# Performance work log

Hardware: AMD Instinct MI355X
Metric: run time of the kernel (lower is better)

## Reference

```python
import jax, jax.numpy as jnp
import numpy as np

N_NODES = 100000
N_EDGES = 1000000
IN_DIM, HID_DIM, OUT_DIM = 64, 64, 128


def gcn_conv(x, W, b, src, dst, deg_inv_sqrt, n_nodes):
    # PyG GCNConv: x' = D^{-1/2} (A + I) D^{-1/2} (x W) + b
    xw = x @ W  # [N, out]
    norm = deg_inv_sqrt[src] * deg_inv_sqrt[dst]  # [E'] (edges incl. self-loops)
    msgs = xw[src] * norm[:, None]  # gather + scale, [E', out]
    out = jax.ops.segment_sum(msgs, dst, num_segments=n_nodes)
    return out + b


def setup_inputs() -> dict:
    key = jax.random.key(0)
    ks = jax.random.split(key, 8)
    x = jax.random.normal(ks[0], (N_NODES, IN_DIM), dtype=jnp.float32)
    edge_index = jax.random.randint(ks[1], (2, N_EDGES), 0, N_NODES, dtype=jnp.int64 if jax.config.read('jax_enable_x64') else jnp.int32)
    # Glorot-ish init for weights, zeros for biases (matches GCNConv defaults)
    def glorot(k, fan_in, fan_out):
        s = jnp.sqrt(6.0 / (fan_in + fan_out))
        return jax.random.uniform(k, (fan_in, fan_out), jnp.float32, -s, s)
    return {
        "x": x,
        "W1": glorot(ks[2], IN_DIM, HID_DIM), "b1": jnp.zeros((HID_DIM,), jnp.float32),
        "W2": glorot(ks[3], HID_DIM, HID_DIM), "b2": jnp.zeros((HID_DIM,), jnp.float32),
        "W3": glorot(ks[4], HID_DIM, OUT_DIM), "b3": jnp.zeros((OUT_DIM,), jnp.float32),
        "edge_index": edge_index,
    }


def reference(x, W1, b1, W2, b2, W3, b3, edge_index):
    n = x.shape[0]
    loop = jnp.arange(n, dtype=edge_index.dtype)
    src = jnp.concatenate([edge_index[0], loop])  # add self-loops
    dst = jnp.concatenate([edge_index[1], loop])
    deg = jax.ops.segment_sum(jnp.ones_like(dst, dtype=x.dtype), dst, num_segments=n)
    deg_inv_sqrt = jnp.where(deg > 0, jax.lax.rsqrt(deg), 0.0)
    # Dropout(p=0.5) is identity in eval mode
    h = jax.nn.relu(gcn_conv(x, W1, b1, src, dst, deg_inv_sqrt, n))
    h = jax.nn.relu(gcn_conv(h, W2, b2, src, dst, deg_inv_sqrt, n))
    return gcn_conv(h, W3, b3, src, dst, deg_inv_sqrt, n)
```

## Files before the change

### kernel.cpp

```cpp
#include <hip/hip_runtime.h>
#include <hip/hip_fp16.h>


#define NBMAX 512
#define EPB   4096


__global__ __launch_bounds__(256) void bin_hist(const int* __restrict__ dst,
                                                int* __restrict__ hist, int E, int NB) {
  __shared__ int cnt[NBMAX];
  for (int i = threadIdx.x; i < NB; i += 256) cnt[i] = 0;
  __syncthreads();
  int base = blockIdx.x * EPB;
  for (int it = 0; it < EPB; it += 256) {
    int e = base + it + threadIdx.x;
    if (e < E) atomicAdd(&cnt[dst[e] >> 8], 1);
  }
  __syncthreads();
  for (int i = threadIdx.x; i < NB; i += 256) hist[(size_t)blockIdx.x * NB + i] = cnt[i];
}

__global__ __launch_bounds__(256) void bucket_prefix(int* __restrict__ hist,
                                                     int* __restrict__ bucket_tot,
                                                     int nblk, int NB) {
  __shared__ int tmp[256];
  int b = blockIdx.x;
  int t = threadIdx.x;
  int v = (t < nblk) ? hist[(size_t)t * NB + b] : 0;
  tmp[t] = v;
  __syncthreads();
  for (int off = 1; off < 256; off <<= 1) {
    int a = (t >= off) ? tmp[t - off] : 0;
    __syncthreads();
    tmp[t] += a;
    __syncthreads();
  }
  if (t < nblk) hist[(size_t)t * NB + b] = tmp[t] - v;
  if (t == 255) bucket_tot[b] = tmp[255];
}

__global__ __launch_bounds__(512) void bucket_scan(const int* __restrict__ bucket_tot,
                                                   int* __restrict__ bucket_off, int NB, int E) {
  __shared__ int tmp[NBMAX];
  int t = threadIdx.x;
  int v = (t < NB) ? bucket_tot[t] : 0;
  tmp[t] = v;
  __syncthreads();
  for (int off = 1; off < 512; off <<= 1) {
    int a = (t >= off) ? tmp[t - off] : 0;
    __syncthreads();
    tmp[t] += a;
    __syncthreads();
  }
  if (t < NB) bucket_off[t] = tmp[t] - v;
  if (t == 0) bucket_off[NB] = E;
}

__global__ __launch_bounds__(256) void bin_scatter(const int* __restrict__ src,
                                                   const int* __restrict__ dst,
                                                   const int* __restrict__ chunk_excl,
                                                   const int* __restrict__ bucket_off,
                                                   int* __restrict__ pairs, int E, int NB) {
  __shared__ int cur[NBMAX];
  for (int i = threadIdx.x; i < NB; i += 256)
    cur[i] = bucket_off[i] + chunk_excl[(size_t)blockIdx.x * NB + i];
  __syncthreads();
  int base = blockIdx.x * EPB;
  for (int it = 0; it < EPB; it += 256) {
    int e = base + it + threadIdx.x;
    if (e < E) {
      int d = dst[e];
      int pos = atomicAdd(&cur[d >> 8], 1);
      pairs[pos] = src[e] | ((d & 255) << 17);
    }
  }
}

__device__ __forceinline__ unsigned int packh(float a, float b) {
  unsigned int lo = (unsigned int)__half_as_ushort(__float2half_rn(a));
  unsigned int hi = (unsigned int)__half_as_ushort(__float2half_rn(b));
  return lo | (hi << 16);
}

__device__ __forceinline__ void unpack_add(float& x0, float& x1, unsigned int u) {
  x0 += __half2float(__ushort_as_half((unsigned short)(u & 0xffffu)));
  x1 += __half2float(__ushort_as_half((unsigned short)(u >> 16)));
}

__global__ __launch_bounds__(256) void bucket_fill(const int* __restrict__ pairs,
                                                   const int* __restrict__ bucket_off,
                                                   int* __restrict__ row_ptr,
                                                   int* __restrict__ csr_src,
                                                   float* __restrict__ dis,
                                                   const float* __restrict__ x,
                                                   unsigned short* __restrict__ xs,
                                                   int n, int NB) {
  __shared__ int cnt[256];
  __shared__ int tmp[256];
  __shared__ int cur[256];
  __shared__ float sdis[256];
  int b = blockIdx.x;
  int t = threadIdx.x;
  int node_base = b << 8;
  int ebeg = bucket_off[b];
  int eend = bucket_off[b + 1];
  cnt[t] = 0;
  __syncthreads();
  for (int e = ebeg + t; e < eend; e += 256) {
    atomicAdd(&cnt[(pairs[e] >> 17) & 255], 1);
  }
  __syncthreads();
  int v = cnt[t];
  tmp[t] = v;
  __syncthreads();
  for (int off = 1; off < 256; off <<= 1) {
    int a = (t >= off) ? tmp[t - off] : 0;
    __syncthreads();
    tmp[t] += a;
    __syncthreads();
  }
  int excl = tmp[t] - v;
  int node = node_base + t;
  float s = rsqrtf((float)v + 1.0f);
  sdis[t] = s;
  if (node < n) {
    row_ptr[node] = ebeg + excl;
    dis[node] = s;
  }
  cur[t] = ebeg + excl;
  if (b == NB - 1 && t == 0) row_ptr[n] = eend;
  __syncthreads();
  for (int e = ebeg + t; e < eend; e += 256) {
    int p = pairs[e];
    int pos = atomicAdd(&cur[(p >> 17) & 255], 1);
    csr_src[pos] = p & 0x1FFFF;
  }
  int rows = n - node_base;
  if (rows > 256) rows = 256;
  for (int i = t; i < rows * 8; i += 256) {
    int r = i >> 3;
    float sc = sdis[r];
    const float4* p = (const float4*)(x + ((size_t)(node_base + r) * 64) + (i & 7) * 8);
    float4 f0 = p[0];
    float4 f1 = p[1];
    uint4 u;
    u.x = packh(f0.x * sc, f0.y * sc);
    u.y = packh(f0.z * sc, f0.w * sc);
    u.z = packh(f1.x * sc, f1.y * sc);
    u.w = packh(f1.z * sc, f1.w * sc);
    *(uint4*)(xs + (size_t)(node_base + r) * 64 + (i & 7) * 8) = u;
  }
}


__device__ __forceinline__ void fma4(float4& a, float s, const float4 w) {
  a.x = fmaf(s, w.x, a.x);
  a.y = fmaf(s, w.y, a.y);
  a.z = fmaf(s, w.z, a.z);
  a.w = fmaf(s, w.w, a.w);
}

template <bool RELU, bool SCALE, bool OUTH, int NCB>
__global__ __launch_bounds__(256, 6) void gcn_layer(
    const int* __restrict__ row_ptr, const int* __restrict__ csr_src,
    const unsigned short* __restrict__ in, const float* __restrict__ dis,
    const float* __restrict__ W, const float* __restrict__ Bv,
    float* __restrict__ yF, unsigned short* __restrict__ yH, int n) {
  __shared__ float Xs[64 * 68];
  int tid = threadIdx.x;
  int rb = blockIdx.x * 64;

  int l15 = tid & 15;
  int gbase = tid & 48;
  int grp = tid >> 4;
  for (int it = 0; it < 4; ++it) {
    int r = it * 16 + grp;
    int cl = min(rb + r, n - 1);
    int beg = row_ptr[cl];
    int end = row_ptr[cl + 1];

    float a0 = 0.f, a1 = 0.f, a2 = 0.f, a3 = 0.f;
    {
      uint2 q = *(const uint2*)(in + (size_t)cl * 64 + l15 * 4);
      unpack_add(a0, a1, q.x); unpack_add(a2, a3, q.y);
    }
    int k = beg;
    for (; k + 16 <= end; k += 16) {
      int idx = csr_src[k + l15];
#pragma unroll
      for (int rr = 0; rr < 16; rr += 2) {
        int s0 = __shfl(idx, gbase + rr);
        int s1 = __shfl(idx, gbase + rr + 1);
        uint2 q0 = *(const uint2*)(in + (size_t)s0 * 64 + l15 * 4);
        uint2 q1 = *(const uint2*)(in + (size_t)s1 * 64 + l15 * 4);
        unpack_add(a0, a1, q0.x); unpack_add(a2, a3, q0.y);
        unpack_add(a0, a1, q1.x); unpack_add(a2, a3, q1.y);
      }
    }
    int cnt = end - k;
    if (cnt > 0) {
      int ii = k + l15;
      int last = end - 1;
      ii = (ii < end) ? ii : last;
      int idx = csr_src[ii];
#pragma unroll
      for (int rr = 0; rr < 16; rr += 2) {
        int s0 = __shfl(idx, gbase + rr);
        int s1 = __shfl(idx, gbase + rr + 1);
        uint2 q0 = *(const uint2*)(in + (size_t)s0 * 64 + l15 * 4);
        uint2 q1 = *(const uint2*)(in + (size_t)s1 * 64 + l15 * 4);
        q0.x = (rr < cnt) ? q0.x : 0u;
        q0.y = (rr < cnt) ? q0.y : 0u;
        q1.x = (rr + 1 < cnt) ? q1.x : 0u;
        q1.y = (rr + 1 < cnt) ? q1.y : 0u;
        unpack_add(a0, a1, q0.x); unpack_add(a2, a3, q0.y);
        unpack_add(a0, a1, q1.x); unpack_add(a2, a3, q1.y);
      }
    }
    float sc = dis[cl];
    *(float4*)&Xs[r * 68 + l15 * 4] =
        make_float4(a0 * sc, a1 * sc, a2 * sc, a3 * sc);
  }
  __syncthreads();

  int r0 = (tid >> 4) << 2;
  int c0 = (tid & 15) << 2;
  int gr0 = rb + r0;

#pragma unroll
  for (int cb = 0; cb < NCB; ++cb) {
    float4 a0 = make_float4(0.f, 0.f, 0.f, 0.f);
    float4 a1 = a0, a2 = a0, a3 = a0;
    const float* wbase = W + cb * 64 + c0;

#pragma unroll 2
    for (int kc = 0; kc < 64; kc += 4) {
      float4 x0 = *(const float4*)&Xs[(r0 + 0) * 68 + kc];
      float4 x1 = *(const float4*)&Xs[(r0 + 1) * 68 + kc];
      float4 x2 = *(const float4*)&Xs[(r0 + 2) * 68 + kc];
      float4 x3 = *(const float4*)&Xs[(r0 + 3) * 68 + kc];
      const float* wp = wbase + (size_t)kc * (64 * NCB);
      float4 w0 = *(const float4*)(wp + 0 * (64 * NCB));
      float4 w1 = *(const float4*)(wp + 1 * (64 * NCB));
      float4 w2 = *(const float4*)(wp + 2 * (64 * NCB));
      float4 w3 = *(const float4*)(wp + 3 * (64 * NCB));
      fma4(a0, x0.x, w0); fma4(a0, x0.y, w1); fma4(a0, x0.z, w2); fma4(a0, x0.w, w3);
      fma4(a1, x1.x, w0); fma4(a1, x1.y, w1); fma4(a1, x1.z, w2); fma4(a1, x1.w, w3);
      fma4(a2, x2.x, w0); fma4(a2, x2.y, w1); fma4(a2, x2.z, w2); fma4(a2, x2.w, w3);
      fma4(a3, x3.x, w0); fma4(a3, x3.y, w1); fma4(a3, x3.z, w2); fma4(a3, x3.w, w3);
    }

    float4 bb = *(const float4*)&Bv[cb * 64 + c0];
#pragma unroll
    for (int ri = 0; ri < 4; ++ri) {
      int gr = gr0 + ri;
      if (gr >= n) break;
      float4 v = (ri == 0) ? a0 : (ri == 1) ? a1 : (ri == 2) ? a2 : a3;
      v.x += bb.x; v.y += bb.y; v.z += bb.z; v.w += bb.w;
      if (RELU) {
        v.x = fmaxf(v.x, 0.f); v.y = fmaxf(v.y, 0.f);
        v.z = fmaxf(v.z, 0.f); v.w = fmaxf(v.w, 0.f);
      }
      if (SCALE) {
        float s = dis[gr];
        v.x *= s; v.y *= s; v.z *= s; v.w *= s;
      }
      if (OUTH) {
        uint2 u;
        u.x = packh(v.x, v.y);
        u.y = packh(v.z, v.w);
        *(uint2*)(yH + (size_t)gr * 64 + c0) = u;
      } else {
        *(float4*)&yF[(size_t)gr * (64 * NCB) + cb * 64 + c0] = v;
      }
    }
  }
}


extern "C" void kernel_launch(void* const* d_in, const int* in_sizes, int n_in,
                              void* d_out, int out_size, void* d_ws, size_t ws_size,
                              hipStream_t stream) {
  const float* x  = (const float*)d_in[0];
  const float* W1 = (const float*)d_in[1];
  const float* b1 = (const float*)d_in[2];
  const float* W2 = (const float*)d_in[3];
  const float* b2 = (const float*)d_in[4];
  const float* W3 = (const float*)d_in[5];
  const float* b3 = (const float*)d_in[6];
  const int*   ei = (const int*)d_in[7];

  const int n = in_sizes[0] / 64;
  const int E = in_sizes[7] / 2;
  const int* src = ei;
  const int* dst = ei + E;

  const int NB    = (n + 255) >> 8;
  const int nblkA = (E + EPB - 1) / EPB;

  float* dis = (float*)d_ws;
  unsigned short* bufA = (unsigned short*)(dis + n);
  unsigned short* bufB = bufA + (size_t)n * 64;
  int* row_ptr = (int*)(bufB + (size_t)n * 64);
  int* csr_src = row_ptr + (n + 2);
  int* pairs   = csr_src + E;
  int* hist       = pairs + E;
  int* bucket_tot = hist + (size_t)nblkA * NB;
  int* bucket_off = bucket_tot + NB;
  float* out = (float*)d_out;

  dim3 blk(256);
  int gL = (n + 63) / 64;

  bin_hist<<<nblkA, blk, 0, stream>>>(dst, hist, E, NB);
  bucket_prefix<<<NB, blk, 0, stream>>>(hist, bucket_tot, nblkA, NB);
  bucket_scan<<<1, 512, 0, stream>>>(bucket_tot, bucket_off, NB, E);
  bin_scatter<<<nblkA, blk, 0, stream>>>(src, dst, hist, bucket_off, pairs, E, NB);
  bucket_fill<<<NB, blk, 0, stream>>>(pairs, bucket_off, row_ptr, csr_src, dis, x, bufA, n, NB);

  gcn_layer<true, true, true, 1><<<gL, blk, 0, stream>>>(
      row_ptr, csr_src, bufA, dis, W1, b1, nullptr, bufB, n);

  gcn_layer<true, true, true, 1><<<gL, blk, 0, stream>>>(
      row_ptr, csr_src, bufB, dis, W2, b2, nullptr, bufA, n);

  gcn_layer<false, false, false, 2><<<gL, blk, 0, stream>>>(
      row_ptr, csr_src, bufA, dis, W3, b3, out, nullptr, n);
}
```

Measured before the change: 262.0 us.

## Fuse edge binning into one pass with chunk-local scans; stage weights in LDS

The separate histogram, per-bucket prefix and scatter kernels become a single kernel. Each 4096-edge chunk counts its buckets, scans them locally, writes its pairs into its own chunk region, and adds its counts to global bucket totals atomically. bucket_fill then walks each chunk's slice for its bucket using the stored local offsets. This removes one pass over src/dst and two launches, but the fill loops become serial per thread over short chunk slices, and the pair order becomes nondeterministic. Separately, the GCN layer copies W into shared memory and its occupancy hint drops from 6 to 4.

```diff
diff --git a/kernel.cpp b/kernel.cpp
--- a/kernel.cpp
+++ b/kernel.cpp
@@ -6,37 +6,51 @@
 #define EPB   4096
 
 
-__global__ __launch_bounds__(256) void bin_hist(const int* __restrict__ dst,
-                                                int* __restrict__ hist, int E, int NB) {
+__global__ __launch_bounds__(512) void build_scatter(
+    const int* __restrict__ src, const int* __restrict__ dst,
+    int* __restrict__ bucket_tot, int* __restrict__ locScan,
+    int* __restrict__ pairs, int E, int NB) {
   __shared__ int cnt[NBMAX];
-  for (int i = threadIdx.x; i < NB; i += 256) cnt[i] = 0;
-  __syncthreads();
-  int base = blockIdx.x * EPB;
-  for (int it = 0; it < EPB; it += 256) {
-    int e = base + it + threadIdx.x;
-    if (e < E) atomicAdd(&cnt[dst[e] >> 8], 1);
-  }
-  __syncthreads();
-  for (int i = threadIdx.x; i < NB; i += 256) hist[(size_t)blockIdx.x * NB + i] = cnt[i];
-}
-
-__global__ __launch_bounds__(256) void bucket_prefix(int* __restrict__ hist,
-                                                     int* __restrict__ bucket_tot,
-                                                     int nblk, int NB) {
-  __shared__ int tmp[256];
-  int b = blockIdx.x;
+  __shared__ int tmp[NBMAX];
+  int c = blockIdx.x;
   int t = threadIdx.x;
-  int v = (t < nblk) ? hist[(size_t)t * NB + b] : 0;
+  int base = c * EPB;
+  for (int i = t; i < NB; i += 512) cnt[i] = 0;
+  __syncthreads();
+  int myS[8], myD[8];
+#pragma unroll
+  for (int i = 0; i < 8; ++i) {
+    int e = base + i * 512 + t;
+    bool v = e < E;
+    myS[i] = v ? src[e] : -1;
+    myD[i] = v ? dst[e] : 0;
+    if (v) atomicAdd(&cnt[myD[i] >> 8], 1);
+  }
+  __syncthreads();
+  if (t < NB) atomicAdd(&bucket_tot[t], cnt[t]);
+  int v = (t < NB) ? cnt[t] : 0;
   tmp[t] = v;
   __syncthreads();
-  for (int off = 1; off < 256; off <<= 1) {
+  for (int off = 1; off < 512; off <<= 1) {
     int a = (t >= off) ? tmp[t - off] : 0;
     __syncthreads();
     tmp[t] += a;
     __syncthreads();
   }
-  if (t < nblk) hist[(size_t)t * NB + b] = tmp[t] - v;
-  if (t == 255) bucket_tot[b] = tmp[255];
+  int excl = tmp[t] - v;
+  size_t lsBase = (size_t)c * (NB + 1);
+  if (t < NB) locScan[lsBase + t] = excl;
+  if (t == NB - 1) locScan[lsBase + NB] = tmp[t];
+  __syncthreads();
+  if (t < NB) cnt[t] = excl;
+  __syncthreads();
+#pragma unroll
+  for (int i = 0; i < 8; ++i) {
+    if (myS[i] >= 0) {
+      int pos = atomicAdd(&cnt[myD[i] >> 8], 1);
+      pairs[base + pos] = myS[i] | ((myD[i] & 255) << 17);
+    }
+  }
 }
 
 __global__ __launch_bounds__(512) void bucket_scan(const int* __restrict__ bucket_tot,
@@ -56,26 +70,6 @@
   if (t == 0) bucket_off[NB] = E;
 }
 
-__global__ __launch_bounds__(256) void bin_scatter(const int* __restrict__ src,
-                                                   const int* __restrict__ dst,
-                                                   const int* __restrict__ chunk_excl,
-                                                   const int* __restrict__ bucket_off,
-                                                   int* __restrict__ pairs, int E, int NB) {
-  __shared__ int cur[NBMAX];
-  for (int i = threadIdx.x; i < NB; i += 256)
-    cur[i] = bucket_off[i] + chunk_excl[(size_t)blockIdx.x * NB + i];
-  __syncthreads();
-  int base = blockIdx.x * EPB;
-  for (int it = 0; it < EPB; it += 256) {
-    int e = base + it + threadIdx.x;
-    if (e < E) {
-      int d = dst[e];
-      int pos = atomicAdd(&cur[d >> 8], 1);
-      pairs[pos] = src[e] | ((d & 255) << 17);
-    }
-  }
-}
-
 __device__ __forceinline__ unsigned int packh(float a, float b) {
   unsigned int lo = (unsigned int)__half_as_ushort(__float2half_rn(a));
   unsigned int hi = (unsigned int)__half_as_ushort(__float2half_rn(b));
@@ -88,13 +82,14 @@
 }
 
 __global__ __launch_bounds__(256) void bucket_fill(const int* __restrict__ pairs,
+                                                   const int* __restrict__ locScan,
                                                    const int* __restrict__ bucket_off,
                                                    int* __restrict__ row_ptr,
                                                    int* __restrict__ csr_src,
                                                    float* __restrict__ dis,
                                                    const float* __restrict__ x,
                                                    unsigned short* __restrict__ xs,
-                                                   int n, int NB) {
+                                                   int n, int NB, int nchunk) {
   __shared__ int cnt[256];
   __shared__ int tmp[256];
   __shared__ int cur[256];
@@ -106,8 +101,11 @@
   int eend = bucket_off[b + 1];
   cnt[t] = 0;
   __syncthreads();
-  for (int e = ebeg + t; e < eend; e += 256) {
-    atomicAdd(&cnt[(pairs[e] >> 17) & 255], 1);
+  for (int c = t; c < nchunk; c += 256) {
+    int s = locScan[(size_t)c * (NB + 1) + b];
+    int e = locScan[(size_t)c * (NB + 1) + b + 1];
+    const int* pp = pairs + (size_t)c * EPB;
+    for (int i = s; i < e; ++i) atomicAdd(&cnt[(pp[i] >> 17) & 255], 1);
   }
   __syncthreads();
   int v = cnt[t];
@@ -130,10 +128,15 @@
   cur[t] = ebeg + excl;
   if (b == NB - 1 && t == 0) row_ptr[n] = eend;
   __syncthreads();
-  for (int e = ebeg + t; e < eend; e += 256) {
-    int p = pairs[e];
-    int pos = atomicAdd(&cur[(p >> 17) & 255], 1);
-    csr_src[pos] = p & 0x1FFFF;
+  for (int c = t; c < nchunk; c += 256) {
+    int sE = locScan[(size_t)c * (NB + 1) + b];
+    int eE = locScan[(size_t)c * (NB + 1) + b + 1];
+    const int* pp = pairs + (size_t)c * EPB;
+    for (int i = sE; i < eE; ++i) {
+      int p = pp[i];
+      int pos = atomicAdd(&cur[(p >> 17) & 255], 1);
+      csr_src[pos] = p & 0x1FFFF;
+    }
   }
   int rows = n - node_base;
   if (rows > 256) rows = 256;
@@ -161,14 +164,21 @@
 }
 
 template <bool RELU, bool SCALE, bool OUTH, int NCB>
-__global__ __launch_bounds__(256, 6) void gcn_layer(
+__global__ __launch_bounds__(256, 4) void gcn_layer(
     const int* __restrict__ row_ptr, const int* __restrict__ csr_src,
     const unsigned short* __restrict__ in, const float* __restrict__ dis,
     const float* __restrict__ W, const float* __restrict__ Bv,
     float* __restrict__ yF, unsigned short* __restrict__ yH, int n) {
   __shared__ float Xs[64 * 68];
+  __shared__ float Ws[64 * 64 * NCB];
   int tid = threadIdx.x;
   int rb = blockIdx.x * 64;
+
+  for (int i = tid; i < 64 * 16 * NCB; i += 256) {
+    int k = i / (16 * NCB);
+    int cq = (i % (16 * NCB)) << 2;
+    *(float4*)&Ws[k * (64 * NCB) + cq] = *(const float4*)&W[(size_t)k * (64 * NCB) + cq];
+  }
 
   int l15 = tid & 15;
   int gbase = tid & 48;
@@ -231,7 +241,6 @@
   for (int cb = 0; cb < NCB; ++cb) {
     float4 a0 = make_float4(0.f, 0.f, 0.f, 0.f);
     float4 a1 = a0, a2 = a0, a3 = a0;
-    const float* wbase = W + cb * 64 + c0;
 
 #pragma unroll 2
     for (int kc = 0; kc < 64; kc += 4) {
@@ -239,7 +248,7 @@
       float4 x1 = *(const float4*)&Xs[(r0 + 1) * 68 + kc];
       float4 x2 = *(const float4*)&Xs[(r0 + 2) * 68 + kc];
       float4 x3 = *(const float4*)&Xs[(r0 + 3) * 68 + kc];
-      const float* wp = wbase + (size_t)kc * (64 * NCB);
+      const float* wp = &Ws[(size_t)kc * (64 * NCB) + cb * 64 + c0];
       float4 w0 = *(const float4*)(wp + 0 * (64 * NCB));
       float4 w1 = *(const float4*)(wp + 1 * (64 * NCB));
       float4 w2 = *(const float4*)(wp + 2 * (64 * NCB));
@@ -304,19 +313,19 @@
   int* row_ptr = (int*)(bufB + (size_t)n * 64);
   int* csr_src = row_ptr + (n + 2);
   int* pairs   = csr_src + E;
-  int* hist       = pairs + E;
-  int* bucket_tot = hist + (size_t)nblkA * NB;
+  int* locScan = pairs + E;
+  int* bucket_tot = locScan + (size_t)nblkA * (NB + 1);
   int* bucket_off = bucket_tot + NB;
   float* out = (float*)d_out;
 
   dim3 blk(256);
   int gL = (n + 63) / 64;
 
-  bin_hist<<<nblkA, blk, 0, stream>>>(dst, hist, E, NB);
-  bucket_prefix<<<NB, blk, 0, stream>>>(hist, bucket_tot, nblkA, NB);
+  hipMemsetAsync(bucket_tot, 0, (size_t)NB * sizeof(int), stream);
+  build_scatter<<<nblkA, 512, 0, stream>>>(src, dst, bucket_tot, locScan, pairs, E, NB);
   bucket_scan<<<1, 512, 0, stream>>>(bucket_tot, bucket_off, NB, E);
-  bin_scatter<<<nblkA, blk, 0, stream>>>(src, dst, hist, bucket_off, pairs, E, NB);
-  bucket_fill<<<NB, blk, 0, stream>>>(pairs, bucket_off, row_ptr, csr_src, dis, x, bufA, n, NB);
+  bucket_fill<<<NB, blk, 0, stream>>>(pairs, locScan, bucket_off, row_ptr, csr_src,
+                                      dis, x, bufA, n, NB, nblkA);
 
   gcn_layer<true, true, true, 1><<<gL, blk, 0, stream>>>(
       row_ptr, csr_src, bufA, dis, W1, b1, nullptr, bufB, n);
```

Result: no change. 258.1 us (-1.5%).
